# Kernel tuning notes

Measured on AMD Instinct MI355X. Metric: run time of the kernel, lower is better.

## Reference

```python
import jax, jax.numpy as jnp
import numpy as np

D_MODEL, D_STATE, EXPAND, V, BATCH, L = 32, 16, 2, 19, 32, 256
D_INNER = EXPAND * D_MODEL          # 64
DT_RANK = 2                          # ceil(d_model/16)
N_NODES = BATCH * V                  # 608


def setup_inputs() -> dict:
    key = jax.random.key(0)
    ks = jax.random.split(key, 16)
    # 32 fully-connected directed 19-vertex graphs (no self loops), block-diagonal batching
    ii, jj = np.nonzero(~np.eye(V, dtype=bool))
    offs = (np.arange(BATCH) * V)[:, None]
    src = (ii[None, :] + offs).reshape(-1)
    dst = (jj[None, :] + offs).reshape(-1)
    edge_index = jnp.asarray(np.stack([src, dst]), dtype=jnp.int32)  # (2, 10944)
    E = edge_index.shape[1]
    # dt_proj bias init (inverse softplus of dt in [dt_min, dt_max]), as in the torch module
    dt = jnp.exp(jax.random.uniform(ks[6], (D_INNER,)) * (np.log(0.1) - np.log(0.001)) + np.log(0.001))
    dt = jnp.maximum(dt, 1e-4)
    inv_dt = dt + jnp.log(-jnp.expm1(-dt))
    s = 0.05
    return {
        'x_in': jax.random.normal(ks[0], (N_NODES, L, D_MODEL), jnp.float32),
        'edge_index': edge_index,
        'edge_weight': jax.random.uniform(ks[1], (E,), jnp.float32, 0.1, 1.0),
        'in_proj_w': jax.random.normal(ks[2], (2 * D_INNER, D_MODEL), jnp.float32) * s,
        'x_proj_w': jax.random.normal(ks[3], (DT_RANK + 2 * D_STATE, D_INNER), jnp.float32) * s,
        'dt_proj_w': jax.random.uniform(ks[4], (D_INNER, DT_RANK), jnp.float32, -DT_RANK ** -0.5, DT_RANK ** -0.5),
        'dt_proj_b': inv_dt,
        'A_log': jnp.log(jnp.broadcast_to(jnp.arange(1, D_STATE + 1, dtype=jnp.float32), (D_INNER, D_STATE))),
        'D_param': jnp.ones((D_INNER,), jnp.float32),
        'out_proj_w': jax.random.normal(ks[5], (D_MODEL, D_INNER), jnp.float32) * s,
        'gA_w': jax.random.normal(ks[7], (D_INNER, D_INNER), jnp.float32) * s,
        'gA_b': jnp.zeros((D_INNER,), jnp.float32),
        'gB_w': jax.random.normal(ks[8], (D_INNER, D_INNER), jnp.float32) * s,
        'gB_b': jnp.zeros((D_INNER,), jnp.float32),
        'gC_w': jax.random.normal(ks[9], (D_INNER, D_INNER), jnp.float32) * s,
        'gC_b': jnp.zeros((D_INNER,), jnp.float32),
    }


def reference(x_in, edge_index, edge_weight, in_proj_w, x_proj_w, dt_proj_w,
              dt_proj_b, A_log, D_param, out_proj_w,
              gA_w, gA_b, gB_w, gB_b, gC_w, gC_b):
    n_nodes, seqlen, _ = x_in.shape
    dt_rank = dt_proj_w.shape[1]
    d_state = A_log.shape[1]

    # --- GCN symmetric normalization with self loops (weight 1), as in PyG GCNConv ---
    loop = jnp.arange(n_nodes, dtype=edge_index.dtype)
    src = jnp.concatenate([edge_index[0], loop])
    dst = jnp.concatenate([edge_index[1], loop])
    w = jnp.concatenate([edge_weight, jnp.ones((n_nodes,), edge_weight.dtype)])
    deg = jax.ops.segment_sum(w, dst, num_segments=n_nodes)
    dinv = jax.lax.rsqrt(jnp.maximum(deg, 1e-12))
    norm = w * dinv[src] * dinv[dst]  # (E+n,)

    def gcn_vec(f, W, b):  # f: (V, d)
        h = f @ W.T
        return jax.ops.segment_sum(norm[:, None] * h[src], dst, num_segments=n_nodes) + b

    def gcn_state(f, W, b):  # f: (V, d, n); linear acts on the d (feature) axis
        h = jnp.einsum('vdn,ed->ven', f, W)
        agg = jax.ops.segment_sum(norm[:, None, None] * h[src], dst, num_segments=n_nodes)
        return agg + b[None, :, None]

    # --- projections ---
    xz = jnp.einsum('vld,ed->vle', x_in, in_proj_w)            # (V, L, 2*d_inner)
    x, z = jnp.split(xz, 2, axis=-1)                           # (V, L, d_inner)
    x_dbl = jnp.einsum('vld,ed->vle', x, x_proj_w)
    dtr, Bm, Cm = jnp.split(x_dbl, [dt_rank, dt_rank + d_state], axis=-1)
    dt = jax.nn.softplus(jnp.einsum('vlr,dr->vld', dtr, dt_proj_w) + dt_proj_b)  # (V, L, d_inner)
    A = -jnp.exp(A_log)                                        # (d_inner, d_state)

    # --- selective scan with per-timestep GCN on state (A), input (B), output (C) ---
    def step(s, inp):
        dt_t, B_t, C_t, u_t, z_t = inp  # (V,d), (V,n), (V,n), (V,d), (V,d)
        dA = jnp.exp(dt_t[:, :, None] * A[None])               # (V, d, n)
        sA = gcn_state(s, gA_w, gA_b)
        uB = gcn_vec(u_t, gB_w, gB_b)                          # (V, d)
        s_new = sA * dA + uB[:, :, None] * (dt_t[:, :, None] * B_t[:, None, :])
        sC = gcn_state(s_new, gC_w, gC_b)
        y_t = jnp.einsum('vdn,vn->vd', sC, C_t) + D_param * u_t
        y_t = y_t * jax.nn.silu(z_t)
        return s_new, y_t

    xs = (dt.transpose(1, 0, 2), Bm.transpose(1, 0, 2), Cm.transpose(1, 0, 2),
          x.transpose(1, 0, 2), z.transpose(1, 0, 2))
    s0 = jnp.zeros((n_nodes, A_log.shape[0], d_state), x_in.dtype)
    _, ys = jax.lax.scan(step, s0, xs)                         # (L, V, d_inner)
    y = ys.transpose(1, 0, 2)                                  # (V, L, d_inner)
    return jnp.einsum('vle,oe->vlo', y, out_proj_w)            # (V, L, d_model)
```

## Files before the change

kernel.cpp:

```cpp
#include <hip/hip_runtime.h>
#include <hip/hip_bf16.h>

typedef __hip_bfloat16 bf16;
typedef unsigned short ushort_t;
typedef __attribute__((ext_vector_type(8))) short bf16x8;
typedef __attribute__((ext_vector_type(4))) float f32x4;

#define NV_   19
#define NB_   32
#define NN_   608
#define LL_   256
#define NE_   10944
#define NEPG  342
#define NROWS (NN_*LL_)
#define NTOT  (NROWS*64)
#define NBC   (NROWS*16)

__device__ __forceinline__ float b2f(bf16 x){ return __bfloat162float(x); }
__device__ __forceinline__ bf16 f2b(float x){ return __float2bfloat16(x); }
__device__ __forceinline__ unsigned short f2bs(float x){
  union { float f; unsigned u; } c; c.f = x;
  unsigned r = c.u + 0x7FFFu + ((c.u >> 16) & 1u);
  return (unsigned short)(r >> 16);
}
__device__ __forceinline__ float busf(unsigned short s){
  union { unsigned u; float f; } c; c.u = ((unsigned)s) << 16; return c.f;
}
__device__ __forceinline__ unsigned pkrn(float a, float b){
  union { __hip_bfloat162 h2; unsigned u; } c;
  float2 t; t.x = a; t.y = b;
  c.h2 = __float22bfloat162_rn(t);
  return c.u;
}
__device__ __forceinline__ float blo(unsigned u){
  union { unsigned x; float f; } c; c.x = u << 16; return c.f;
}
__device__ __forceinline__ float bhi(unsigned u){
  union { unsigned x; float f; } c; c.x = u & 0xffff0000u; return c.f;
}
__device__ __forceinline__ float softplusf(float x){
  return fmaxf(x, 0.f) + log1pf(expf(-fabsf(x)));
}

__global__ __launch_bounds__(384)
void k_gcn(const float* __restrict__ ew, float* __restrict__ Mg){
  __shared__ float ewL[NEPG];
  __shared__ float dinvL[NV_];
  int b = blockIdx.x, tid = threadIdx.x;
  if (tid < NEPG) ewL[tid] = ew[b*NEPG + tid];
  __syncthreads();
  if (tid < NV_){
    float s = 1.0f;
    #pragma unroll
    for (int i = 0; i < NV_; i++){
      if (i == tid) continue;
      s += ewL[i*18 + (tid < i ? tid : tid - 1)];
    }
    dinvL[tid] = rsqrtf(fmaxf(s, 1e-12f));
  }
  __syncthreads();
  if (tid < 361){
    int j = tid / NV_, i = tid - j*NV_;
    float m;
    if (i == j){ float r = dinvL[j]; m = r*r; }
    else        m = ewL[i*18 + (j < i ? j : j - 1)] * dinvL[i] * dinvL[j];
    Mg[b*361 + tid] = m;
  }
}

__global__ __launch_bounds__(256)
void k_proj(const float* __restrict__ xin, const float* __restrict__ inw,
            const float* __restrict__ xpw,
            bf16* __restrict__ u, bf16* __restrict__ zs,
            float* __restrict__ dtr, bf16* __restrict__ Bm, bf16* __restrict__ Cm){
  __shared__ float inT[32*129];
  __shared__ float xpT[64*35];
  __shared__ float xl[2][4][32];
  __shared__ float xh[2][4][64];
  int tid = threadIdx.x;
  for (int i = tid; i < 128*32; i += 256){
    int e = i >> 5, d = i & 31;
    inT[d*129 + e] = inw[i];
  }
  for (int i = tid; i < 34*64; i += 256){
    int j = i >> 6, e = i & 63;
    xpT[e*35 + j] = xpw[i];
  }
  int w = tid >> 6, lane = tid & 63;
  for (int rg = 0; rg < 32; rg++){
    int p = rg & 1;
    int r = (blockIdx.x*32 + rg)*4 + w;
    if (lane < 32) xl[p][w][lane] = xin[r*32 + lane];
    __syncthreads();
    float a0 = 0.f, a1 = 0.f;
    #pragma unroll
    for (int d = 0; d < 32; d++){
      float xv = xl[p][w][d];
      a0 = fmaf(inT[d*129 + lane], xv, a0);
      a1 = fmaf(inT[d*129 + 64 + lane], xv, a1);
    }
    int node = r >> 8, l = r & 255;
    long ob = (long)l*NN_ + node;
    u[ob*64 + lane] = f2b(a0);
    zs[ob*64 + lane] = f2b(a1 / (1.f + expf(-a1)));
    xh[p][w][lane] = a0;
    __syncthreads();
    if (lane < 34){
      float acc = 0.f;
      #pragma unroll
      for (int e = 0; e < 64; e++) acc = fmaf(xpT[e*35 + lane], xh[p][w][e], acc);
      if (lane < 2)       dtr[ob*2 + lane] = acc;
      else if (lane < 18) Bm[ob*16 + lane - 2] = f2b(acc);
      else                Cm[ob*16 + lane - 18] = f2b(acc);
    }
  }
}

__global__ __launch_bounds__(256)
void k_ub(const bf16* __restrict__ u, const float* __restrict__ gBw,
          const float* __restrict__ gBb, const float* __restrict__ Mg,
          const float* __restrict__ dtrg, const float* __restrict__ dtw,
          const float* __restrict__ dtb,
          bf16* __restrict__ uBsp, bf16* __restrict__ spb){
  __shared__ float wT[64*65];
  __shared__ float uL[19*64];
  __shared__ float hL[20*64];
  __shared__ float MLP[640];
  int b = blockIdx.x & 31, tc = blockIdx.x >> 5;
  int tid = threadIdx.x;
  for (int i = tid; i < 4096; i += 256){
    int e = i >> 6, d = i & 63;
    wT[d*65 + e] = gBw[i];
  }
  for (int i = tid; i < 640; i += 256){
    int vp = i >> 5, c = i & 31, g = c >> 3, k = c & 7;
    int v = g + 4*k;
    MLP[i] = (k < 5 && vp < 19 && v < 19) ? Mg[b*361 + v*19 + vp] : 0.f;
  }
  int vg = tid >> 6, e = tid & 63;
  int v0 = vg, v1 = vg+4, v2 = vg+8, v3 = vg+12, v4 = vg+16;
  int v4c = (vg == 3) ? 18 : v4;
  float w0e = dtw[e*2], w1e = dtw[e*2 + 1], dbe = dtb[e], bbe = gBb[e];
  const float* mlb = MLP + vg*8;
  for (int tt = 0; tt < 8; tt++){
    int t = tc*8 + tt;
    long rb = (long)t*NN_ + b*19;
    const bf16* up = u + rb*64;
    for (int i = tid; i < 1216; i += 256) uL[i] = b2f(up[i]);
    __syncthreads();
    float h0=0.f,h1=0.f,h2=0.f,h3=0.f,h4=0.f;
    #pragma unroll
    for (int d = 0; d < 64; d++){
      float wv = wT[d*65 + e];
      h0 = fmaf(wv, uL[v0*64 + d], h0);
      h1 = fmaf(wv, uL[v1*64 + d], h1);
      h2 = fmaf(wv, uL[v2*64 + d], h2);
      h3 = fmaf(wv, uL[v3*64 + d], h3);
      h4 = fmaf(wv, uL[v4c*64 + d], h4);
    }
    hL[v0*64 + e] = h0; hL[v1*64 + e] = h1; hL[v2*64 + e] = h2;
    hL[v3*64 + e] = h3; hL[v4*64 + e] = h4;
    __syncthreads();
    float acc0=bbe, acc1=bbe, acc2=bbe, acc3=bbe, acc4=bbe;
    #pragma unroll
    for (int vp = 0; vp < 20; vp++){
      float hv = hL[vp*64 + e];
      float4 m4 = *(const float4*)(mlb + vp*32);
      float  m5 = mlb[vp*32 + 4];
      acc0 = fmaf(m4.x, hv, acc0); acc1 = fmaf(m4.y, hv, acc1);
      acc2 = fmaf(m4.z, hv, acc2); acc3 = fmaf(m4.w, hv, acc3);
      acc4 = fmaf(m5,  hv, acc4);
    }
    float2 q0 = *(const float2*)(dtrg + (rb+v0)*2);
    float2 q1 = *(const float2*)(dtrg + (rb+v1)*2);
    float2 q2 = *(const float2*)(dtrg + (rb+v2)*2);
    float2 q3 = *(const float2*)(dtrg + (rb+v3)*2);
    float2 q4 = *(const float2*)(dtrg + (rb+v4c)*2);
    float s0 = softplusf(fmaf(q0.x, w0e, fmaf(q0.y, w1e, dbe)));
    float s1 = softplusf(fmaf(q1.x, w0e, fmaf(q1.y, w1e, dbe)));
    float s2 = softplusf(fmaf(q2.x, w0e, fmaf(q2.y, w1e, dbe)));
    float s3 = softplusf(fmaf(q3.x, w0e, fmaf(q3.y, w1e, dbe)));
    float s4 = softplusf(fmaf(q4.x, w0e, fmaf(q4.y, w1e, dbe)));
    bf16* op = uBsp + rb*64;
    bf16* sp = spb + rb*64;
    op[v0*64 + e] = f2b(acc0*s0);  sp[v0*64 + e] = f2b(s0);
    op[v1*64 + e] = f2b(acc1*s1);  sp[v1*64 + e] = f2b(s1);
    op[v2*64 + e] = f2b(acc2*s2);  sp[v2*64 + e] = f2b(s2);
    op[v3*64 + e] = f2b(acc3*s3);  sp[v3*64 + e] = f2b(s3);
    if (vg != 3){ op[v4*64 + e] = f2b(acc4*s4); sp[v4*64 + e] = f2b(s4); }
    __syncthreads();
  }
}

__global__ __launch_bounds__(1024)
void k_scan(const float* __restrict__ Mg,
            const bf16* __restrict__ spbg, const bf16* __restrict__ uBspg,
            const bf16* __restrict__ Bg, const bf16* __restrict__ Cg,
            const float* __restrict__ gAw, const float* __restrict__ gAb,
            const float* __restrict__ gCw, const float* __restrict__ gCb,
            const float* __restrict__ Alog, bf16* __restrict__ yp)
{
  __shared__ __align__(16) short Sb[2*32*72];
  __shared__ __align__(16) short H0[2*64*40];
  __shared__ __align__(16) short H1[2*64*40];
  __shared__ __align__(16) short Yx[2][32*68];
  int d_ = blockIdx.x;
  int b = (d_ & 7) | ((d_ >> 6) << 3);
  int npair = (d_ >> 3) & 7;
  int tid = threadIdx.x;
  int team = tid >> 9;
  int tw   = (tid >> 6) & 7;
  int lane = tid & 63;
  int l15  = lane & 15, quad = lane >> 4;
  int n = npair*2 + team;
  int mt = tw >> 2, nt = tw & 3;
  int et = tw >> 1, vt = tw & 1;

  for (int i = tid; i < 2304; i += 1024) ((int*)Sb)[i] = 0;

  bf16x8 wa0, wa1, wc0, wc1;
  {
    #define PACK8(dst, p) { float4 lo_ = *(const float4*)(p); \
      float4 hi_ = *(const float4*)((p)+4); \
      dst[0]=(short)f2bs(lo_.x); dst[1]=(short)f2bs(lo_.y); \
      dst[2]=(short)f2bs(lo_.z); dst[3]=(short)f2bs(lo_.w); \
      dst[4]=(short)f2bs(hi_.x); dst[5]=(short)f2bs(hi_.y); \
      dst[6]=(short)f2bs(hi_.z); dst[7]=(short)f2bs(hi_.w); }
    const float* wrA = gAw + (16*nt + l15)*64 + quad*8;
    const float* wrC = gCw + (16*nt + l15)*64 + quad*8;
    PACK8(wa0, wrA) PACK8(wa1, wrA + 32)
    PACK8(wc0, wrC) PACK8(wc1, wrC + 32)
    #undef PACK8
  }
  bf16x8 mf;
  {
    const float* mb = Mg + b*361;
    int vr = 16*vt + l15; if (vr > 18) vr = 18;
    #pragma unroll
    for (int j = 0; j < 8; j++){
      int vp = quad*8 + j;
      mf[j] = (short)f2bs((vp < 19) ? mb[vr*19 + vp] : 0.f);
    }
  }
  int e0 = 16*et + 4*quad;
  int v_ = 16*vt + l15;
  int vc = (v_ > 18) ? 18 : v_;
  bool vok = (v_ < 19);
  float4 gab = *(const float4*)(gAb + e0);
  float4 gcb = *(const float4*)(gCb + e0);
  float An0 = -__expf(Alog[(e0+0)*16 + n]);
  float An1 = -__expf(Alog[(e0+1)*16 + n]);
  float An2 = -__expf(Alog[(e0+2)*16 + n]);
  float An3 = -__expf(Alog[(e0+3)*16 + n]);

  short* Sme  = Sb + team*32*72;
  short* H0me = H0 + team*64*40;
  short* H1me = H1 + team*64*40;
  int nodeBase = b*19;
  const short* prS  = Sme + (16*mt + l15)*72 + quad*8;
  short*       pwH0 = H0me + (16*nt + l15)*40 + 16*mt + quad*4;
  short*       pwH1 = H1me + (16*nt + l15)*40 + 16*mt + quad*4;
  const short* arH0 = H0me + (16*et + l15)*40 + quad*8;
  const short* arH1 = H1me + (16*et + l15)*40 + quad*8;
  short*       swS  = Sme + v_*72 + e0;

  long row0 = (long)nodeBase + vc;
  const ushort_t* psp = (const ushort_t*)spbg  + row0*64 + e0;
  const ushort_t* pub = (const ushort_t*)uBspg + row0*64 + e0;
  const ushort_t* pB  = (const ushort_t*)Bg + row0*16 + n;
  const ushort_t* pC  = (const ushort_t*)Cg + row0*16 + n;
  uint2 sp_n = *(const uint2*)psp;
  uint2 ub_n = *(const uint2*)pub;
  float B_n = busf(*pB);
  float C_b2 = busf(*pC);
  float C_a = 0.f;
  float pyo0=0.f,pyo1=0.f,pyo2=0.f,pyo3=0.f;
  float pyn0=0.f,pyn1=0.f,pyn2=0.f,pyn3=0.f;

  __syncthreads();
  {
    bf16x8 a0 = *(const bf16x8*)prS;
    bf16x8 a1 = *(const bf16x8*)(prS + 32);
    f32x4 p = {0.f,0.f,0.f,0.f};
    p = __builtin_amdgcn_mfma_f32_16x16x32_bf16(a0, wa0, p, 0,0,0);
    p = __builtin_amdgcn_mfma_f32_16x16x32_bf16(a1, wa1, p, 0,0,0);
    uint2 h; h.x = pkrn(p[0], p[1]); h.y = pkrn(p[2], p[3]);
    *(uint2*)pwH0 = h;
  }
  __syncthreads();

  for (int t = 0; t < 256; t++){
    uint2 sp_u = sp_n, ub_u = ub_n; float B_u = B_n;
    psp += NN_*64; pub += NN_*64; pB += NN_*16; pC += NN_*16;
    sp_n = *(const uint2*)psp;
    ub_n = *(const uint2*)pub;
    B_n = busf(*pB);
    float C_t = busf(*pC);
    bf16x8 hf0 = *(const bf16x8*)arH0;
    bf16x8 hf1 = *(const bf16x8*)arH1;
    {
      f32x4 qa = {gab.x, gab.y, gab.z, gab.w};
      qa = __builtin_amdgcn_mfma_f32_16x16x32_bf16(hf0, mf, qa, 0,0,0);
      float dA0 = __expf(blo(sp_u.x)*An0);
      float dA1 = __expf(bhi(sp_u.x)*An1);
      float dA2 = __expf(blo(sp_u.y)*An2);
      float dA3 = __expf(bhi(sp_u.y)*An3);
      float x0 = fmaf(qa[0], dA0, blo(ub_u.x)*B_u);
      float x1 = fmaf(qa[1], dA1, bhi(ub_u.x)*B_u);
      float x2 = fmaf(qa[2], dA2, blo(ub_u.y)*B_u);
      float x3 = fmaf(qa[3], dA3, bhi(ub_u.y)*B_u);
      uint2 sv; sv.x = pkrn(x0, x1); sv.y = pkrn(x2, x3);
      *(uint2*)swS = sv;
    }
    if (team == 0 && t >= 2 && vok){
      uint2 yv = *(const uint2*)(&Yx[t & 1][v_*68 + e0]);
      uint2 ov;
      ov.x = pkrn(pyo0 + blo(yv.x), pyo1 + bhi(yv.x));
      ov.y = pkrn(pyo2 + blo(yv.y), pyo3 + bhi(yv.y));
      *(uint2*)(yp + (((long)npair*256 + (t-2))*NN_ + nodeBase + v_)*64 + e0) = ov;
    }
    if (t >= 1){
      f32x4 qc = {gcb.x, gcb.y, gcb.z, gcb.w};
      qc = __builtin_amdgcn_mfma_f32_16x16x32_bf16(hf1, mf, qc, 0,0,0);
      float y0 = qc[0]*C_a, y1 = qc[1]*C_a, y2 = qc[2]*C_a, y3 = qc[3]*C_a;
      if (team == 1){
        uint2 yv; yv.x = pkrn(y0, y1); yv.y = pkrn(y2, y3);
        *(uint2*)(&Yx[(t-1) & 1][v_*68 + e0]) = yv;
      } else {
        pyo0 = pyn0; pyo1 = pyn1; pyo2 = pyn2; pyo3 = pyn3;
        pyn0 = y0; pyn1 = y1; pyn2 = y2; pyn3 = y3;
      }
    }
    C_a = C_b2; C_b2 = C_t;
    __syncthreads();
    {
      bf16x8 a0 = *(const bf16x8*)prS;
      bf16x8 a1 = *(const bf16x8*)(prS + 32);
      f32x4 p = {0.f,0.f,0.f,0.f};
      p = __builtin_amdgcn_mfma_f32_16x16x32_bf16(a0, wc0, p, 0,0,0);
      p = __builtin_amdgcn_mfma_f32_16x16x32_bf16(a1, wc1, p, 0,0,0);
      uint2 h; h.x = pkrn(p[0], p[1]); h.y = pkrn(p[2], p[3]);
      *(uint2*)pwH1 = h;
      f32x4 r = {0.f,0.f,0.f,0.f};
      r = __builtin_amdgcn_mfma_f32_16x16x32_bf16(a0, wa0, r, 0,0,0);
      r = __builtin_amdgcn_mfma_f32_16x16x32_bf16(a1, wa1, r, 0,0,0);
      uint2 g; g.x = pkrn(r[0], r[1]); g.y = pkrn(r[2], r[3]);
      *(uint2*)pwH0 = g;
    }
    __syncthreads();
  }
  {
    bf16x8 hf1 = *(const bf16x8*)arH1;
    f32x4 qc = {gcb.x, gcb.y, gcb.z, gcb.w};
    qc = __builtin_amdgcn_mfma_f32_16x16x32_bf16(hf1, mf, qc, 0,0,0);
    float y0 = qc[0]*C_a, y1 = qc[1]*C_a, y2 = qc[2]*C_a, y3 = qc[3]*C_a;
    if (team == 1){
      uint2 yv; yv.x = pkrn(y0, y1); yv.y = pkrn(y2, y3);
      *(uint2*)(&Yx[1][v_*68 + e0]) = yv;
    } else {
      pyo0 = pyn0; pyo1 = pyn1; pyo2 = pyn2; pyo3 = pyn3;
      pyn0 = y0; pyn1 = y1; pyn2 = y2; pyn3 = y3;
    }
  }
  __syncthreads();
  if (team == 0 && vok){
    uint2 yv = *(const uint2*)(&Yx[0][v_*68 + e0]);
    uint2 ov;
    ov.x = pkrn(pyo0 + blo(yv.x), pyo1 + bhi(yv.x));
    ov.y = pkrn(pyo2 + blo(yv.y), pyo3 + bhi(yv.y));
    *(uint2*)(yp + (((long)npair*256 + 254)*NN_ + nodeBase + v_)*64 + e0) = ov;
    uint2 yw = *(const uint2*)(&Yx[1][v_*68 + e0]);
    uint2 o2;
    o2.x = pkrn(pyn0 + blo(yw.x), pyn1 + bhi(yw.x));
    o2.y = pkrn(pyn2 + blo(yw.y), pyn3 + bhi(yw.y));
    *(uint2*)(yp + (((long)npair*256 + 255)*NN_ + nodeBase + v_)*64 + e0) = o2;
  }
}

__global__ __launch_bounds__(256)
void k_final(const bf16* __restrict__ yp, const bf16* __restrict__ u,
             const bf16* __restrict__ zs, const float* __restrict__ Dp,
             const float* __restrict__ ow, float* __restrict__ out)
{
  __shared__ float oT[64*33];
  __shared__ float yl[16*68];
  int tid = threadIdx.x;
  for (int i = tid; i < 32*64; i += 256){
    int o = i >> 6, e = i & 63;
    oT[e*33 + o] = ow[i];
  }
  int w = tid >> 6, lane = tid & 63;
  int rl = w*4 + (lane >> 4);
  int e4 = (lane & 15)*4;
  float4 dp4 = *(const float4*)(Dp + e4);
  int o = tid & 31, rp = tid >> 5;
  for (int it = 0; it < 4; it++){
    long row = (long)blockIdx.x*64 + it*16 + rl;
    long base = row*64 + e4;
    uint2 uv = *(const uint2*)((const ushort_t*)u + base);
    uint2 zv = *(const uint2*)((const ushort_t*)zs + base);
    float y0 = dp4.x * blo(uv.x), y1 = dp4.y * bhi(uv.x);
    float y2 = dp4.z * blo(uv.y), y3 = dp4.w * bhi(uv.y);
    #pragma unroll
    for (int q = 0; q < 8; q++){
      uint2 pv = *(const uint2*)((const ushort_t*)yp + (long)q*NTOT + base);
      y0 += blo(pv.x); y1 += bhi(pv.x);
      y2 += blo(pv.y); y3 += bhi(pv.y);
    }
    y0 *= blo(zv.x); y1 *= bhi(zv.x); y2 *= blo(zv.y); y3 *= bhi(zv.y);
    float4 yv4; yv4.x = y0; yv4.y = y1; yv4.z = y2; yv4.w = y3;
    *(float4*)(&yl[rl*68 + e4]) = yv4;
    __syncthreads();
    #pragma unroll
    for (int h = 0; h < 2; h++){
      int r2 = rp + h*8;
      float acc = 0.f;
      #pragma unroll
      for (int e = 0; e < 64; e++) acc = fmaf(oT[e*33 + o], yl[r2*68 + e], acc);
      long rr = (long)blockIdx.x*64 + it*16 + r2;
      int t = (int)(rr / NN_), node = (int)(rr - (long)t*NN_);
      out[((long)node*256 + t)*32 + o] = acc;
    }
    __syncthreads();
  }
}

extern "C" void kernel_launch(void* const* d_in, const int* in_sizes, int n_in,
                              void* d_out, int out_size, void* d_ws, size_t ws_size,
                              hipStream_t stream)
{
  (void)in_sizes; (void)n_in; (void)out_size; (void)ws_size;
  const float* xin = (const float*)d_in[0];
  const int*   ei  = (const int*)  d_in[1];
  const float* ew  = (const float*)d_in[2];
  const float* inw = (const float*)d_in[3];
  const float* xpw = (const float*)d_in[4];
  const float* dtw = (const float*)d_in[5];
  const float* dtb = (const float*)d_in[6];
  const float* Alog= (const float*)d_in[7];
  const float* Dp  = (const float*)d_in[8];
  const float* ow  = (const float*)d_in[9];
  const float* gAw = (const float*)d_in[10];
  const float* gAb = (const float*)d_in[11];
  const float* gBw = (const float*)d_in[12];
  const float* gBb = (const float*)d_in[13];
  const float* gCw = (const float*)d_in[14];
  const float* gCb = (const float*)d_in[15];
  float* out = (float*)d_out;
  (void)ei;

  float* Mg   = (float*)d_ws;
  float* deg  = Mg + 11552;
  float* dinv = deg + 608;
  float* dtr  = dinv + 608;
  bf16*  u    = (bf16*)(dtr + 2*NROWS);
  bf16*  zs   = u + NTOT;
  bf16*  uBsp = zs + NTOT;
  bf16*  Bm   = uBsp + NTOT;
  bf16*  Cm   = Bm + NBC;
  bf16*  spb  = Cm + NBC;
  bf16*  yp   = spb + NTOT;

  k_gcn  <<<NB_, 384, 0, stream>>>(ew, Mg);
  k_proj <<<NROWS/(4*32), 256, 0, stream>>>(xin, inw, xpw, u, zs, dtr, Bm, Cm);
  k_ub   <<<32*32, 256, 0, stream>>>(u, gBw, gBb, Mg, dtr, dtw, dtb, uBsp, spb);
  k_scan <<<NB_*8, 1024, 0, stream>>>(Mg, spb, uBsp, Bm, Cm, gAw, gAb, gCw, gCb,
                                      Alog, yp);
  k_final<<<NROWS/(4*16), 256, 0, stream>>>(yp, u, zs, Dp, ow, out);
}
```

Measured before the change: 633.5 us.

## Split scan into one block per state index when workspace allows

Adds a k_scan16 variant that runs one 512-thread block per (graph, state index), so two state indices no longer share a block and their partial outputs no longer need to be combined through shared memory. Each block writes its own partial-y slice, and k_final is templated to sum 16 partial buffers instead of 8. The new path is chosen only when the workspace is large enough. It doubles the partial-output memory traffic in exchange for twice as many blocks and less in-loop coordination. The original two-team kernel remains as the fallback.

```diff
diff --git a/kernel.cpp b/kernel.cpp
--- a/kernel.cpp
+++ b/kernel.cpp
@@ -192,31 +192,29 @@
   }
 }
 
-__global__ __launch_bounds__(1024)
-void k_scan(const float* __restrict__ Mg,
-            const bf16* __restrict__ spbg, const bf16* __restrict__ uBspg,
-            const bf16* __restrict__ Bg, const bf16* __restrict__ Cg,
-            const float* __restrict__ gAw, const float* __restrict__ gAb,
-            const float* __restrict__ gCw, const float* __restrict__ gCb,
-            const float* __restrict__ Alog, bf16* __restrict__ yp)
+__global__ __launch_bounds__(512)
+void k_scan16(const float* __restrict__ Mg,
+              const bf16* __restrict__ spbg, const bf16* __restrict__ uBspg,
+              const bf16* __restrict__ Bg, const bf16* __restrict__ Cg,
+              const float* __restrict__ gAw, const float* __restrict__ gAb,
+              const float* __restrict__ gCw, const float* __restrict__ gCb,
+              const float* __restrict__ Alog, bf16* __restrict__ yp)
 {
-  __shared__ __align__(16) short Sb[2*32*72];
-  __shared__ __align__(16) short H0[2*64*40];
-  __shared__ __align__(16) short H1[2*64*40];
-  __shared__ __align__(16) short Yx[2][32*68];
+  __shared__ __align__(16) short Sme[32*72];
+  __shared__ __align__(16) short H0me[64*40];
+  __shared__ __align__(16) short H1me[64*40];
   int d_ = blockIdx.x;
-  int b = (d_ & 7) | ((d_ >> 6) << 3);
-  int npair = (d_ >> 3) & 7;
+  int b = (d_ & 7) | ((d_ >> 7) << 3);
+  int n = (d_ >> 3) & 15;
   int tid = threadIdx.x;
-  int team = tid >> 9;
-  int tw   = (tid >> 6) & 7;
+  int tw   = tid >> 6;
   int lane = tid & 63;
   int l15  = lane & 15, quad = lane >> 4;
-  int n = npair*2 + team;
   int mt = tw >> 2, nt = tw & 3;
   int et = tw >> 1, vt = tw & 1;
 
-  for (int i = tid; i < 2304; i += 1024) ((int*)Sb)[i] = 0;
+  for (int i = tid; i < 1152; i += 512) ((int*)Sme)[i] = 0;
+  for (int i = tid; i < 1280; i += 512) ((int*)H0me)[i] = 0;
 
   bf16x8 wa0, wa1, wc0, wc1;
   {
@@ -253,9 +251,6 @@
   float An2 = -__expf(Alog[(e0+2)*16 + n]);
   float An3 = -__expf(Alog[(e0+3)*16 + n]);
 
-  short* Sme  = Sb + team*32*72;
-  short* H0me = H0 + team*64*40;
-  short* H1me = H1 + team*64*40;
   int nodeBase = b*19;
   const short* prS  = Sme + (16*mt + l15)*72 + quad*8;
   short*       pwH0 = H0me + (16*nt + l15)*40 + 16*mt + quad*4;
@@ -274,19 +269,8 @@
   float B_n = busf(*pB);
   float C_b2 = busf(*pC);
   float C_a = 0.f;
-  float pyo0=0.f,pyo1=0.f,pyo2=0.f,pyo3=0.f;
-  float pyn0=0.f,pyn1=0.f,pyn2=0.f,pyn3=0.f;
-
-  __syncthreads();
-  {
-    bf16x8 a0 = *(const bf16x8*)prS;
-    bf16x8 a1 = *(const bf16x8*)(prS + 32);
-    f32x4 p = {0.f,0.f,0.f,0.f};
-    p = __builtin_amdgcn_mfma_f32_16x16x32_bf16(a0, wa0, p, 0,0,0);
-    p = __builtin_amdgcn_mfma_f32_16x16x32_bf16(a1, wa1, p, 0,0,0);
-    uint2 h; h.x = pkrn(p[0], p[1]); h.y = pkrn(p[2], p[3]);
-    *(uint2*)pwH0 = h;
-  }
+  bf16* py = yp + (((long)n*256)*NN_ + nodeBase + v_)*64 + e0;
+
   __syncthreads();
 
   for (int t = 0; t < 256; t++){
@@ -312,24 +296,16 @@
       uint2 sv; sv.x = pkrn(x0, x1); sv.y = pkrn(x2, x3);
       *(uint2*)swS = sv;
     }
-    if (team == 0 && t >= 2 && vok){
-      uint2 yv = *(const uint2*)(&Yx[t & 1][v_*68 + e0]);
-      uint2 ov;
-      ov.x = pkrn(pyo0 + blo(yv.x), pyo1 + bhi(yv.x));
-      ov.y = pkrn(pyo2 + blo(yv.y), pyo3 + bhi(yv.y));
-      *(uint2*)(yp + (((long)npair*256 + (t-2))*NN_ + nodeBase + v_)*64 + e0) = ov;
-    }
     if (t >= 1){
       f32x4 qc = {gcb.x, gcb.y, gcb.z, gcb.w};
       qc = __builtin_amdgcn_mfma_f32_16x16x32_bf16(hf1, mf, qc, 0,0,0);
-      float y0 = qc[0]*C_a, y1 = qc[1]*C_a, y2 = qc[2]*C_a, y3 = qc[3]*C_a;
-      if (team == 1){
-        uint2 yv; yv.x = pkrn(y0, y1); yv.y = pkrn(y2, y3);
-        *(uint2*)(&Yx[(t-1) & 1][v_*68 + e0]) = yv;
-      } else {
-        pyo0 = pyn0; pyo1 = pyn1; pyo2 = pyn2; pyo3 = pyn3;
-        pyn0 = y0; pyn1 = y1; pyn2 = y2; pyn3 = y3;
+      if (vok){
+        uint2 yv;
+        yv.x = pkrn(qc[0]*C_a, qc[1]*C_a);
+        yv.y = pkrn(qc[2]*C_a, qc[3]*C_a);
+        *(uint2*)py = yv;
       }
+      py += (long)NN_*64;
     }
     C_a = C_b2; C_b2 = C_t;
     __syncthreads();
@@ -353,6 +329,176 @@
     bf16x8 hf1 = *(const bf16x8*)arH1;
     f32x4 qc = {gcb.x, gcb.y, gcb.z, gcb.w};
     qc = __builtin_amdgcn_mfma_f32_16x16x32_bf16(hf1, mf, qc, 0,0,0);
+    if (vok){
+      uint2 yv;
+      yv.x = pkrn(qc[0]*C_a, qc[1]*C_a);
+      yv.y = pkrn(qc[2]*C_a, qc[3]*C_a);
+      *(uint2*)py = yv;
+    }
+  }
+}
+
+__global__ __launch_bounds__(1024)
+void k_scan8(const float* __restrict__ Mg,
+             const bf16* __restrict__ spbg, const bf16* __restrict__ uBspg,
+             const bf16* __restrict__ Bg, const bf16* __restrict__ Cg,
+             const float* __restrict__ gAw, const float* __restrict__ gAb,
+             const float* __restrict__ gCw, const float* __restrict__ gCb,
+             const float* __restrict__ Alog, bf16* __restrict__ yp)
+{
+  __shared__ __align__(16) short Sb[2*32*72];
+  __shared__ __align__(16) short H0[2*64*40];
+  __shared__ __align__(16) short H1[2*64*40];
+  __shared__ __align__(16) short Yx[2][32*68];
+  int d_ = blockIdx.x;
+  int b = (d_ & 7) | ((d_ >> 6) << 3);
+  int npair = (d_ >> 3) & 7;
+  int tid = threadIdx.x;
+  int team = tid >> 9;
+  int tw   = (tid >> 6) & 7;
+  int lane = tid & 63;
+  int l15  = lane & 15, quad = lane >> 4;
+  int n = npair*2 + team;
+  int mt = tw >> 2, nt = tw & 3;
+  int et = tw >> 1, vt = tw & 1;
+
+  for (int i = tid; i < 2304; i += 1024) ((int*)Sb)[i] = 0;
+
+  bf16x8 wa0, wa1, wc0, wc1;
+  {
+    #define PACK8(dst, p) { float4 lo_ = *(const float4*)(p); \
+      float4 hi_ = *(const float4*)((p)+4); \
+      dst[0]=(short)f2bs(lo_.x); dst[1]=(short)f2bs(lo_.y); \
+      dst[2]=(short)f2bs(lo_.z); dst[3]=(short)f2bs(lo_.w); \
+      dst[4]=(short)f2bs(hi_.x); dst[5]=(short)f2bs(hi_.y); \
+      dst[6]=(short)f2bs(hi_.z); dst[7]=(short)f2bs(hi_.w); }
+    const float* wrA = gAw + (16*nt + l15)*64 + quad*8;
+    const float* wrC = gCw + (16*nt + l15)*64 + quad*8;
+    PACK8(wa0, wrA) PACK8(wa1, wrA + 32)
+    PACK8(wc0, wrC) PACK8(wc1, wrC + 32)
+    #undef PACK8
+  }
+  bf16x8 mf;
+  {
+    const float* mb = Mg + b*361;
+    int vr = 16*vt + l15; if (vr > 18) vr = 18;
+    #pragma unroll
+    for (int j = 0; j < 8; j++){
+      int vp = quad*8 + j;
+      mf[j] = (short)f2bs((vp < 19) ? mb[vr*19 + vp] : 0.f);
+    }
+  }
+  int e0 = 16*et + 4*quad;
+  int v_ = 16*vt + l15;
+  int vc = (v_ > 18) ? 18 : v_;
+  bool vok = (v_ < 19);
+  float4 gab = *(const float4*)(gAb + e0);
+  float4 gcb = *(const float4*)(gCb + e0);
+  float An0 = -__expf(Alog[(e0+0)*16 + n]);
+  float An1 = -__expf(Alog[(e0+1)*16 + n]);
+  float An2 = -__expf(Alog[(e0+2)*16 + n]);
+  float An3 = -__expf(Alog[(e0+3)*16 + n]);
+
+  short* Sme  = Sb + team*32*72;
+  short* H0me = H0 + team*64*40;
+  short* H1me = H1 + team*64*40;
+  int nodeBase = b*19;
+  const short* prS  = Sme + (16*mt + l15)*72 + quad*8;
+  short*       pwH0 = H0me + (16*nt + l15)*40 + 16*mt + quad*4;
+  short*       pwH1 = H1me + (16*nt + l15)*40 + 16*mt + quad*4;
+  const short* arH0 = H0me + (16*et + l15)*40 + quad*8;
+  const short* arH1 = H1me + (16*et + l15)*40 + quad*8;
+  short*       swS  = Sme + v_*72 + e0;
+
+  long row0 = (long)nodeBase + vc;
+  const ushort_t* psp = (const ushort_t*)spbg  + row0*64 + e0;
+  const ushort_t* pub = (const ushort_t*)uBspg + row0*64 + e0;
+  const ushort_t* pB  = (const ushort_t*)Bg + row0*16 + n;
+  const ushort_t* pC  = (const ushort_t*)Cg + row0*16 + n;
+  uint2 sp_n = *(const uint2*)psp;
+  uint2 ub_n = *(const uint2*)pub;
+  float B_n = busf(*pB);
+  float C_b2 = busf(*pC);
+  float C_a = 0.f;
+  float pyo0=0.f,pyo1=0.f,pyo2=0.f,pyo3=0.f;
+  float pyn0=0.f,pyn1=0.f,pyn2=0.f,pyn3=0.f;
+
+  __syncthreads();
+  {
+    bf16x8 a0 = *(const bf16x8*)prS;
+    bf16x8 a1 = *(const bf16x8*)(prS + 32);
+    f32x4 p = {0.f,0.f,0.f,0.f};
+    p = __builtin_amdgcn_mfma_f32_16x16x32_bf16(a0, wa0, p, 0,0,0);
+    p = __builtin_amdgcn_mfma_f32_16x16x32_bf16(a1, wa1, p, 0,0,0);
+    uint2 h; h.x = pkrn(p[0], p[1]); h.y = pkrn(p[2], p[3]);
+    *(uint2*)pwH0 = h;
+  }
+  __syncthreads();
+
+  for (int t = 0; t < 256; t++){
+    uint2 sp_u = sp_n, ub_u = ub_n; float B_u = B_n;
+    psp += NN_*64; pub += NN_*64; pB += NN_*16; pC += NN_*16;
+    sp_n = *(const uint2*)psp;
+    ub_n = *(const uint2*)pub;
+    B_n = busf(*pB);
+    float C_t = busf(*pC);
+    bf16x8 hf0 = *(const bf16x8*)arH0;
+    bf16x8 hf1 = *(const bf16x8*)arH1;
+    {
+      f32x4 qa = {gab.x, gab.y, gab.z, gab.w};
+      qa = __builtin_amdgcn_mfma_f32_16x16x32_bf16(hf0, mf, qa, 0,0,0);
+      float dA0 = __expf(blo(sp_u.x)*An0);
+      float dA1 = __expf(bhi(sp_u.x)*An1);
+      float dA2 = __expf(blo(sp_u.y)*An2);
+      float dA3 = __expf(bhi(sp_u.y)*An3);
+      float x0 = fmaf(qa[0], dA0, blo(ub_u.x)*B_u);
+      float x1 = fmaf(qa[1], dA1, bhi(ub_u.x)*B_u);
+      float x2 = fmaf(qa[2], dA2, blo(ub_u.y)*B_u);
+      float x3 = fmaf(qa[3], dA3, bhi(ub_u.y)*B_u);
+      uint2 sv; sv.x = pkrn(x0, x1); sv.y = pkrn(x2, x3);
+      *(uint2*)swS = sv;
+    }
+    if (team == 0 && t >= 2 && vok){
+      uint2 yv = *(const uint2*)(&Yx[t & 1][v_*68 + e0]);
+      uint2 ov;
+      ov.x = pkrn(pyo0 + blo(yv.x), pyo1 + bhi(yv.x));
+      ov.y = pkrn(pyo2 + blo(yv.y), pyo3 + bhi(yv.y));
+      *(uint2*)(yp + (((long)npair*256 + (t-2))*NN_ + nodeBase + v_)*64 + e0) = ov;
+    }
+    if (t >= 1){
+      f32x4 qc = {gcb.x, gcb.y, gcb.z, gcb.w};
+      qc = __builtin_amdgcn_mfma_f32_16x16x32_bf16(hf1, mf, qc, 0,0,0);
+      float y0 = qc[0]*C_a, y1 = qc[1]*C_a, y2 = qc[2]*C_a, y3 = qc[3]*C_a;
+      if (team == 1){
+        uint2 yv; yv.x = pkrn(y0, y1); yv.y = pkrn(y2, y3);
+        *(uint2*)(&Yx[(t-1) & 1][v_*68 + e0]) = yv;
+      } else {
+        pyo0 = pyn0; pyo1 = pyn1; pyo2 = pyn2; pyo3 = pyn3;
+        pyn0 = y0; pyn1 = y1; pyn2 = y2; pyn3 = y3;
+      }
+    }
+    C_a = C_b2; C_b2 = C_t;
+    __syncthreads();
+    {
+      bf16x8 a0 = *(const bf16x8*)prS;
+      bf16x8 a1 = *(const bf16x8*)(prS + 32);
+      f32x4 p = {0.f,0.f,0.f,0.f};
+      p = __builtin_amdgcn_mfma_f32_16x16x32_bf16(a0, wc0, p, 0,0,0);
+      p = __builtin_amdgcn_mfma_f32_16x16x32_bf16(a1, wc1, p, 0,0,0);
+      uint2 h; h.x = pkrn(p[0], p[1]); h.y = pkrn(p[2], p[3]);
+      *(uint2*)pwH1 = h;
+      f32x4 r = {0.f,0.f,0.f,0.f};
+      r = __builtin_amdgcn_mfma_f32_16x16x32_bf16(a0, wa0, r, 0,0,0);
+      r = __builtin_amdgcn_mfma_f32_16x16x32_bf16(a1, wa1, r, 0,0,0);
+      uint2 g; g.x = pkrn(r[0], r[1]); g.y = pkrn(r[2], r[3]);
+      *(uint2*)pwH0 = g;
+    }
+    __syncthreads();
+  }
+  {
+    bf16x8 hf1 = *(const bf16x8*)arH1;
+    f32x4 qc = {gcb.x, gcb.y, gcb.z, gcb.w};
+    qc = __builtin_amdgcn_mfma_f32_16x16x32_bf16(hf1, mf, qc, 0,0,0);
     float y0 = qc[0]*C_a, y1 = qc[1]*C_a, y2 = qc[2]*C_a, y3 = qc[3]*C_a;
     if (team == 1){
       uint2 yv; yv.x = pkrn(y0, y1); yv.y = pkrn(y2, y3);
@@ -377,6 +523,7 @@
   }
 }
 
+template<int NQ>
 __global__ __launch_bounds__(256)
 void k_final(const bf16* __restrict__ yp, const bf16* __restrict__ u,
              const bf16* __restrict__ zs, const float* __restrict__ Dp,
@@ -402,7 +549,7 @@
     float y0 = dp4.x * blo(uv.x), y1 = dp4.y * bhi(uv.x);
     float y2 = dp4.z * blo(uv.y), y3 = dp4.w * bhi(uv.y);
     #pragma unroll
-    for (int q = 0; q < 8; q++){
+    for (int q = 0; q < NQ; q++){
       uint2 pv = *(const uint2*)((const ushort_t*)yp + (long)q*NTOT + base);
       y0 += blo(pv.x); y1 += bhi(pv.x);
       y2 += blo(pv.y); y3 += bhi(pv.y);
@@ -429,7 +576,7 @@
                               void* d_out, int out_size, void* d_ws, size_t ws_size,
                               hipStream_t stream)
 {
-  (void)in_sizes; (void)n_in; (void)out_size; (void)ws_size;
+  (void)in_sizes; (void)n_in; (void)out_size;
   const float* xin = (const float*)d_in[0];
   const int*   ei  = (const int*)  d_in[1];
   const float* ew  = (const float*)d_in[2];
@@ -461,10 +608,19 @@
   bf16*  spb  = Cm + NBC;
   bf16*  yp   = spb + NTOT;
 
+  const size_t need16 = 409716608ULL;
+  const bool big = (ws_size == 0) ? false : (ws_size >= need16);
+
   k_gcn  <<<NB_, 384, 0, stream>>>(ew, Mg);
   k_proj <<<NROWS/(4*32), 256, 0, stream>>>(xin, inw, xpw, u, zs, dtr, Bm, Cm);
   k_ub   <<<32*32, 256, 0, stream>>>(u, gBw, gBb, Mg, dtr, dtw, dtb, uBsp, spb);
-  k_scan <<<NB_*8, 1024, 0, stream>>>(Mg, spb, uBsp, Bm, Cm, gAw, gAb, gCw, gCb,
-                                      Alog, yp);
-  k_final<<<NROWS/(4*16), 256, 0, stream>>>(yp, u, zs, Dp, ow, out);
-}
+  if (big){
+    k_scan16<<<NB_*16, 512, 0, stream>>>(Mg, spb, uBsp, Bm, Cm, gAw, gAb,
+                                         gCw, gCb, Alog, yp);
+    k_final<16><<<NROWS/(4*16), 256, 0, stream>>>(yp, u, zs, Dp, ow, out);
+  } else {
+    k_scan8<<<NB_*8, 1024, 0, stream>>>(Mg, spb, uBsp, Bm, Cm, gAw, gAb,
+                                        gCw, gCb, Alog, yp);
+    k_final<8><<<NROWS/(4*16), 256, 0, stream>>>(yp, u, zs, Dp, ow, out);
+  }
+}
```

Result: no change. 631.5 us (-0.3%).
